# Kernel optimization log

Hardware: AMD Instinct MI355X
Metric: run time of the kernel (lower is better)

Reference implementation:

```python
import jax, jax.numpy as jnp
import numpy as np

N_NODES = 100000
N_EDGES = 3200000
HID = 32
N_LAYERS = 3
EDGE_DIM = 2
NODE_IN = 2          # [P, Q]
V_DIM = 2            # [V_mag, V_angle]
VH = V_DIM + HID     # 34, per-node feature fed to the GNN layer
MSG_IN = 2 * VH + EDGE_DIM   # 70
UPD_IN = VH + HID            # 66


def setup_inputs() -> dict:
    key = jax.random.key(0)
    ks = jax.random.split(key, 16)
    s = lambda *sh: 1.0 / np.sqrt(sh[-2]) if len(sh) >= 2 else 0.0
    inp = {
        "P_Q_inj": jax.random.normal(ks[0], (N_NODES, NODE_IN), dtype=jnp.float32),
        "senders": jax.random.randint(ks[1], (N_EDGES,), 0, N_NODES, dtype=jnp.int32),
        "receivers": jax.random.randint(ks[2], (N_EDGES,), 0, N_NODES, dtype=jnp.int32),
        "edge_features": jax.random.normal(ks[3], (N_EDGES, EDGE_DIM), dtype=jnp.float32),
        "edge_mask": jax.random.uniform(ks[4], (N_EDGES,), dtype=jnp.float32),
        # input embedding Dense(hidden_dim)
        "W_in": jax.random.normal(ks[5], (NODE_IN, HID), dtype=jnp.float32) * s(NODE_IN, HID),
        "b_in": jnp.zeros((HID,), dtype=jnp.float32),
        # per-layer params (flax compact loop -> distinct params per layer), stacked on axis 0
        "W_msg": jax.random.normal(ks[6], (N_LAYERS, MSG_IN, HID), dtype=jnp.float32) * s(MSG_IN, HID),
        "b_msg": jnp.zeros((N_LAYERS, HID), dtype=jnp.float32),
        "W_upd": jax.random.normal(ks[7], (N_LAYERS, UPD_IN, HID), dtype=jnp.float32) * s(UPD_IN, HID),
        "b_upd": jnp.zeros((N_LAYERS, HID), dtype=jnp.float32),
        "W_delta": jax.random.normal(ks[8], (N_LAYERS, HID, V_DIM), dtype=jnp.float32) * s(HID, V_DIM),
        "b_delta": jnp.zeros((N_LAYERS, V_DIM), dtype=jnp.float32),
    }
    return inp


def _layer(v, senders, receivers, edge_features, edge_mask, W_msg, b_msg, W_upd, b_upd):
    # v: [N, VH] node features. Gather sender/receiver feats, edge-wise MLP message,
    # soft mask, scatter-sum to receivers, then dense node update.
    msg_in = jnp.concatenate([v[senders], v[receivers], edge_features], axis=-1)  # [E, 70]
    m = jax.nn.relu(msg_in @ W_msg + b_msg)                                       # [E, H]
    m = m * edge_mask[:, None]
    agg = jax.ops.segment_sum(m, receivers, num_segments=v.shape[0])              # [N, H]
    v_out = jnp.concatenate([v, agg], axis=-1) @ W_upd + b_upd                    # [N, H]
    return v_out


def reference(P_Q_inj, senders, receivers, edge_features, edge_mask,
              W_in, b_in, W_msg, b_msg, W_upd, b_upd, W_delta, b_delta):
    V_pred = jnp.zeros_like(P_Q_inj).at[:, 0].set(1.0)   # [N, 2]
    h = P_Q_inj @ W_in + b_in                            # [N, H]
    for l in range(N_LAYERS):
        v_input = jnp.concatenate([V_pred, h], axis=-1)  # [N, 34]
        v_out = _layer(v_input, senders, receivers, edge_features, edge_mask,
                       W_msg[l], b_msg[l], W_upd[l], b_upd[l])
        h = jax.nn.relu(v_out)
        delta_V = h @ W_delta[l] + b_delta[l]
        V_pred = V_pred + delta_V
    return V_pred
```

## Files before the change

### kernel.cpp

```cpp
#include <hip/hip_runtime.h>
#include <hip/hip_fp16.h>

#define NN 100000
#define NE 3200000
#define NB 1563
#define NBLK ((NN + 255) / 256)
#define CHUNK 8192
#define NCH 391
#define CAP 4096

typedef float f32x4 __attribute__((ext_vector_type(4)));
typedef unsigned int u32x4 __attribute__((ext_vector_type(4)));

__device__ __forceinline__ float2 h2f2(unsigned int u) {
  __half2 h;
  *reinterpret_cast<unsigned int*>(&h) = u;
  return __half22float2(h);
}
__device__ __forceinline__ unsigned int f2h2(float x, float y) {
  __half2 h = __floats2half2_rn(x, y);
  return *reinterpret_cast<unsigned int*>(&h);
}


__global__ __launch_bounds__(1024) void k_hist(const int* __restrict__ recv, int* __restrict__ histmat) {
  __shared__ int h[NB];
  int t = threadIdx.x, c = blockIdx.x;
  for (int i = t; i < NB; i += 1024) h[i] = 0;
  __syncthreads();
  int start = c * CHUNK;
  int end = min(start + CHUNK, NE);
  for (int i = start + t; i < end; i += 1024)
    atomicAdd(&h[__builtin_nontemporal_load(recv + i) >> 6], 1);
  __syncthreads();
  for (int i = t; i < NB; i += 1024) histmat[c * NB + i] = h[i];
}


__global__ __launch_bounds__(256) void k_scanA(const int* __restrict__ histmat, int* __restrict__ total) {
  int b = blockIdx.x * 256 + threadIdx.x;
  if (b >= NB) return;
  int s = 0;
#pragma unroll 4
  for (int c = 0; c < NCH; c++) s += histmat[c * NB + b];
  total[b] = s;
}


__global__ __launch_bounds__(256) void k_scanB(const int* __restrict__ total, int* __restrict__ boff) {
  __shared__ int ps[256];
  int t = threadIdx.x;
  const int PER = (NB + 255) / 256;
  int v[PER];
  int s = 0;
#pragma unroll
  for (int k = 0; k < PER; k++) {
    int i = t * PER + k;
    v[k] = (i < NB) ? total[i] : 0;
    s += v[k];
  }
  ps[t] = s;
  __syncthreads();
  for (int o = 1; o < 256; o <<= 1) {
    int x = (t >= o) ? ps[t - o] : 0;
    __syncthreads();
    ps[t] += x;
    __syncthreads();
  }
  int run = (t > 0) ? ps[t - 1] : 0;
#pragma unroll
  for (int k = 0; k < PER; k++) {
    int i = t * PER + k;
    if (i < NB) {
      boff[i] = run;
      run += v[k];
    }
  }
  if (t == 255) boff[NB] = ps[255];
}


__global__ __launch_bounds__(256) void k_scanC(int* __restrict__ histmat, const int* __restrict__ boff) {
  int b = blockIdx.x * 256 + threadIdx.x;
  if (b >= NB) return;
  int run = boff[b];
#pragma unroll 4
  for (int c = 0; c < NCH; c++) {
    int v = histmat[c * NB + b];
    histmat[c * NB + b] = run;
    run += v;
  }
}


__global__ __launch_bounds__(1024) void k_scat(const int* __restrict__ send, const int* __restrict__ recv,
                                               const float2* __restrict__ ef, const float* __restrict__ mask,
                                               const int* __restrict__ boffc, float4* __restrict__ sorted) {
  __shared__ float4 stg[CHUNK];
  __shared__ unsigned short bkt[CHUNK];
  __shared__ int ofs[NB];
  __shared__ int cur[NB];
  __shared__ int wsum[16];
  int t = threadIdx.x, c = blockIdx.x;
  int start = c * CHUNK;
  int end = min(start + CHUNK, NE);
  int len = end - start;
  for (int i = t; i < NB; i += 1024) cur[i] = 0;
  __syncthreads();
  for (int i = start + t; i < end; i += 1024)
    atomicAdd(&cur[__builtin_nontemporal_load(recv + i) >> 6], 1);
  __syncthreads();
  int v0 = (2 * t < NB) ? cur[2 * t] : 0;
  int v1 = (2 * t + 1 < NB) ? cur[2 * t + 1] : 0;
  int s = v0 + v1;
  int lane = t & 63, wid = t >> 6;
  for (int o = 1; o < 64; o <<= 1) {
    int x = __shfl_up(s, o);
    if (lane >= o) s += x;
  }
  if (lane == 63) wsum[wid] = s;
  __syncthreads();
  if (wid == 0) {
    int ws = (lane < 16) ? wsum[lane] : 0;
    for (int o = 1; o < 16; o <<= 1) {
      int x = __shfl_up(ws, o);
      if (lane >= o) ws += x;
    }
    if (lane < 16) wsum[lane] = ws;
  }
  __syncthreads();
  int excl = s - v0 - v1 + ((wid > 0) ? wsum[wid - 1] : 0);
  __syncthreads();
  if (2 * t < NB) {
    cur[2 * t] = excl;
    ofs[2 * t] = boffc[c * NB + 2 * t] - excl;
  }
  if (2 * t + 1 < NB) {
    cur[2 * t + 1] = excl + v0;
    ofs[2 * t + 1] = boffc[c * NB + 2 * t + 1] - (excl + v0);
  }
  __syncthreads();
  for (int i = start + t; i < end; i += 1024) {
    int r = recv[i];
    int b = r >> 6;
    int p = atomicAdd(&cur[b], 1);
    float2 e2 = ef[i];
    float4 vv;
    vv.x = __int_as_float((send[i] << 6) | (r & 63));
    vv.y = e2.x;
    vv.z = e2.y;
    vv.w = mask[i];
    stg[p] = vv;
    bkt[p] = (unsigned short)b;
  }
  __syncthreads();
  for (int p = t; p < len; p += 1024) {
    int b = bkt[p];
    sorted[ofs[b] + p] = stg[p];
  }
}


__global__ __launch_bounds__(256) void k_bsort(const int* __restrict__ boff, float4* __restrict__ sorted,
                                               int* __restrict__ row_off) {
  __shared__ int cnt[4096];
  __shared__ int part[256];
  __shared__ float4 stg[CAP];
  int t = threadIdx.x, b = blockIdx.x;
  int base = boff[b], end = boff[b + 1];
  int Eb = end - base;
  int n0 = b * 64;
  for (int i = t; i < 4096; i += 256) cnt[i] = 0;
  __syncthreads();
  for (int e = base + t; e < end; e += 256) {
    int pk = __float_as_int(sorted[e].x);
    int key = ((pk & 63) << 6) | (pk >> 17);
    atomicAdd(&cnt[key], 1);
  }
  __syncthreads();
  int s = 0;
#pragma unroll
  for (int k = 0; k < 16; k++) s += cnt[t * 16 + k];
  part[t] = s;
  __syncthreads();
  for (int o = 1; o < 256; o <<= 1) {
    int x = (t >= o) ? part[t - o] : 0;
    __syncthreads();
    part[t] += x;
    __syncthreads();
  }
  int run = part[t] - s;
#pragma unroll
  for (int k = 0; k < 16; k++) {
    int c = cnt[t * 16 + k];
    cnt[t * 16 + k] = run;
    run += c;
  }
  __syncthreads();
  if (t < 64) {
    int n = n0 + t;
    if (n < NN) row_off[n] = base + cnt[t << 6];
  }
  if (b == NB - 1 && t == 0) row_off[NN] = end;
  __syncthreads();
  for (int e = base + t; e < end; e += 256) {
    float4 r = sorted[e];
    int pk = __float_as_int(r.x);
    int key = ((pk & 63) << 6) | (pk >> 17);
    int p = atomicAdd(&cnt[key], 1);
    stg[p] = r;
  }
  __syncthreads();
  for (int i = t; i < Eb; i += 256) sorted[base + i] = stg[i];
}


__global__ __launch_bounds__(256) void k_init(const float2* __restrict__ PQ,
                                              const float* __restrict__ Win, const float* __restrict__ bin,
                                              const float* __restrict__ Wm, const float* __restrict__ bm,
                                              float* __restrict__ h, __half* __restrict__ a,
                                              float* __restrict__ bp, float2* __restrict__ Vp) {
  int n = blockIdx.x * 256 + threadIdx.x;
  if (n >= NN) return;
  float2 pq = PQ[n];
  float hh[32];
#pragma unroll
  for (int j = 0; j < 32; j++) hh[j] = fmaf(pq.x, Win[j], fmaf(pq.y, Win[32 + j], bin[j]));
  float4* h4 = (float4*)(h + (size_t)n * 32);
#pragma unroll
  for (int j = 0; j < 8; j++) h4[j] = make_float4(hh[4*j], hh[4*j+1], hh[4*j+2], hh[4*j+3]);
  Vp[n] = make_float2(1.0f, 0.0f);
  float av[32], bv[32];
#pragma unroll
  for (int j = 0; j < 32; j++) { av[j] = Wm[j]; bv[j] = Wm[34 * 32 + j] + bm[j]; }
#pragma unroll 1
  for (int k = 0; k < 32; k++) {
    float hk = hh[k];
#pragma unroll
    for (int j = 0; j < 32; j++) {
      av[j] = fmaf(hk, Wm[(2 + k) * 32 + j], av[j]);
      bv[j] = fmaf(hk, Wm[(36 + k) * 32 + j], bv[j]);
    }
  }
  u32x4* dst = (u32x4*)(a + (size_t)n * 32);
#pragma unroll
  for (int g = 0; g < 4; g++) {
    u32x4 p;
    p.x = f2h2(av[g*8+0], av[g*8+1]);
    p.y = f2h2(av[g*8+2], av[g*8+3]);
    p.z = f2h2(av[g*8+4], av[g*8+5]);
    p.w = f2h2(av[g*8+6], av[g*8+7]);
    dst[g] = p;
  }
  float4* b4 = (float4*)(bp + (size_t)n * 32);
#pragma unroll
  for (int j = 0; j < 8; j++) b4[j] = make_float4(bv[4*j], bv[4*j+1], bv[4*j+2], bv[4*j+3]);
}


__global__ __launch_bounds__(256) void k_edge(const __half* __restrict__ a, const float* __restrict__ bp,
                                              const int* __restrict__ row_off, const f32x4* __restrict__ sorted,
                                              const float* __restrict__ Wm, float* __restrict__ agg) {
  int t = threadIdx.x;
  int n = blockIdx.x * 64 + (t >> 2);
  if (n >= NN) return;
  int ch = (t & 3) * 8;
  const float* wr = Wm + 68 * 32 + ch;
  float w0[8], w1[8];
#pragma unroll
  for (int j = 0; j < 8; j++) { w0[j] = wr[j]; w1[j] = wr[32 + j]; }
  const float4 bna = *(const float4*)(bp + (size_t)n * 32 + ch);
  const float4 bnb = *(const float4*)(bp + (size_t)n * 32 + ch + 4);
  float bn[8] = {bna.x, bna.y, bna.z, bna.w, bnb.x, bnb.y, bnb.z, bnb.w};
  float acc[8] = {0.f, 0.f, 0.f, 0.f, 0.f, 0.f, 0.f, 0.f};
  int e0 = row_off[n], e1 = row_off[n + 1];
  f32x4 rec = {0.f, 0.f, 0.f, 0.f};
  if (e0 < e1) rec = __builtin_nontemporal_load(sorted + e0);
#pragma unroll 2
  for (int e = e0; e < e1; ++e) {
    int pk = __float_as_int(rec.x);
    float c0 = rec.y, c1 = rec.z, mk = rec.w;
    const u32x4 pa = *(const u32x4*)(a + (size_t)(pk >> 6) * 32 + ch);
    if (e + 1 < e1) rec = __builtin_nontemporal_load(sorted + e + 1);
    float2 f0 = h2f2(pa.x), f1 = h2f2(pa.y), f2 = h2f2(pa.z), f3 = h2f2(pa.w);
    float av[8] = {f0.x, f0.y, f1.x, f1.y, f2.x, f2.y, f3.x, f3.y};
#pragma unroll
    for (int j = 0; j < 8; j++)
      acc[j] = fmaf(fmaxf(av[j] + fmaf(c0, w0[j], fmaf(c1, w1[j], bn[j])), 0.f), mk, acc[j]);
  }
  float* gp = agg + (size_t)n * 32 + ch;
  *(float4*)gp       = make_float4(acc[0], acc[1], acc[2], acc[3]);
  *(float4*)(gp + 4) = make_float4(acc[4], acc[5], acc[6], acc[7]);
}


__global__ __launch_bounds__(256) void k_node(const float* __restrict__ agg,
                                              const float* __restrict__ Wu, const float* __restrict__ bu,
                                              const float* __restrict__ Wd, const float* __restrict__ bd,
                                              const float* __restrict__ Wm, const float* __restrict__ bm,
                                              float* __restrict__ h, __half* __restrict__ a,
                                              float* __restrict__ bp, float2* __restrict__ Vp,
                                              float2* __restrict__ out, int last) {
  int n = blockIdx.x * 256 + threadIdx.x;
  if (n >= NN) return;
  float2 vp = Vp[n];
  float v0 = vp.x, v1 = vp.y;
  float hh[32], ag[32];
  const float4* h4 = (const float4*)(h + (size_t)n * 32);
  const float4* g4 = (const float4*)(agg + (size_t)n * 32);
#pragma unroll
  for (int jj = 0; jj < 8; jj++) {
    float4 x = h4[jj];
    hh[4*jj] = x.x; hh[4*jj+1] = x.y; hh[4*jj+2] = x.z; hh[4*jj+3] = x.w;
    float4 y = g4[jj];
    ag[4*jj] = y.x; ag[4*jj+1] = y.y; ag[4*jj+2] = y.z; ag[4*jj+3] = y.w;
  }
  float vo[32];
#pragma unroll
  for (int j = 0; j < 32; j++) vo[j] = fmaf(v0, Wu[j], fmaf(v1, Wu[32 + j], bu[j]));
#pragma unroll 1
  for (int k = 0; k < 32; k++) {
    float hk = hh[k], ak = ag[k];
#pragma unroll
    for (int j = 0; j < 32; j++) {
      vo[j] = fmaf(hk, Wu[(2 + k) * 32 + j], vo[j]);
      vo[j] = fmaf(ak, Wu[(34 + k) * 32 + j], vo[j]);
    }
  }
#pragma unroll
  for (int j = 0; j < 32; j++) hh[j] = fmaxf(vo[j], 0.0f);
  float d0 = bd[0], d1 = bd[1];
#pragma unroll 1
  for (int k = 0; k < 32; k++) {
    d0 = fmaf(hh[k], Wd[2 * k], d0);
    d1 = fmaf(hh[k], Wd[2 * k + 1], d1);
  }
  v0 += d0;
  v1 += d1;
  if (last) {
    out[n] = make_float2(v0, v1);
    return;
  }
  Vp[n] = make_float2(v0, v1);
  float4* hw4 = (float4*)(h + (size_t)n * 32);
#pragma unroll
  for (int jj = 0; jj < 8; jj++) hw4[jj] = make_float4(hh[4*jj], hh[4*jj+1], hh[4*jj+2], hh[4*jj+3]);
  float av[32], bv[32];
#pragma unroll
  for (int j = 0; j < 32; j++) {
    av[j] = fmaf(v0, Wm[j], v1 * Wm[32 + j]);
    bv[j] = fmaf(v0, Wm[34 * 32 + j], fmaf(v1, Wm[35 * 32 + j], bm[j]));
  }
#pragma unroll 1
  for (int k = 0; k < 32; k++) {
    float hk = hh[k];
#pragma unroll
    for (int j = 0; j < 32; j++) {
      av[j] = fmaf(hk, Wm[(2 + k) * 32 + j], av[j]);
      bv[j] = fmaf(hk, Wm[(36 + k) * 32 + j], bv[j]);
    }
  }
  u32x4* dst = (u32x4*)(a + (size_t)n * 32);
#pragma unroll
  for (int g = 0; g < 4; g++) {
    u32x4 p;
    p.x = f2h2(av[g*8+0], av[g*8+1]);
    p.y = f2h2(av[g*8+2], av[g*8+3]);
    p.z = f2h2(av[g*8+4], av[g*8+5]);
    p.w = f2h2(av[g*8+6], av[g*8+7]);
    dst[g] = p;
  }
  float4* b4 = (float4*)(bp + (size_t)n * 32);
#pragma unroll
  for (int jj = 0; jj < 8; jj++) b4[jj] = make_float4(bv[4*jj], bv[4*jj+1], bv[4*jj+2], bv[4*jj+3]);
}


extern "C" void kernel_launch(void* const* d_in, const int* in_sizes, int n_in,
                              void* d_out, int out_size, void* d_ws, size_t ws_size,
                              hipStream_t stream) {
  const float* PQ   = (const float*)d_in[0];
  const int*   send = (const int*)d_in[1];
  const int*   recv = (const int*)d_in[2];
  const float* ef   = (const float*)d_in[3];
  const float* mask = (const float*)d_in[4];
  const float* Win  = (const float*)d_in[5];
  const float* bin  = (const float*)d_in[6];
  const float* Wmsg = (const float*)d_in[7];
  const float* bmsg = (const float*)d_in[8];
  const float* Wupd = (const float*)d_in[9];
  const float* bupd = (const float*)d_in[10];
  const float* Wdel = (const float*)d_in[11];
  const float* bdel = (const float*)d_in[12];
  float2* out = (float2*)d_out;

  char* w = (char*)d_ws;
  auto alloc = [&](size_t bytes) {
    char* p = w;
    w += (bytes + 255) & ~(size_t)255;
    return p;
  };
  float4* sorted = (float4*)alloc((size_t)NE * 16);
  int* histmat = (int*)alloc((size_t)NCH * NB * 4);
  int* total   = (int*)alloc((size_t)NB * 4);
  int* boff    = (int*)alloc(((size_t)NB + 1) * 4);
  int* row_off = (int*)alloc(((size_t)NN + 1) * 4);
  float* h    = (float*)alloc((size_t)NN * 32 * 4);
  __half* a   = (__half*)alloc((size_t)NN * 32 * 2);
  float* bp   = (float*)alloc((size_t)NN * 32 * 4);
  float* agg  = (float*)alloc((size_t)NN * 32 * 4);
  float2* Vp  = (float2*)alloc((size_t)NN * 8);

  k_hist<<<NCH, 1024, 0, stream>>>(recv, histmat);
  k_scanA<<<(NB + 255) / 256, 256, 0, stream>>>(histmat, total);
  k_scanB<<<1, 256, 0, stream>>>(total, boff);
  k_scanC<<<(NB + 255) / 256, 256, 0, stream>>>(histmat, boff);
  k_scat<<<NCH, 1024, 0, stream>>>(send, recv, (const float2*)ef, mask, histmat, sorted);
  k_bsort<<<NB, 256, 0, stream>>>(boff, sorted, row_off);

  k_init<<<NBLK, 256, 0, stream>>>((const float2*)PQ, Win, bin, Wmsg, bmsg, h, a, bp, Vp);

  for (int l = 0; l < 3; l++) {
    int last = (l == 2) ? 1 : 0;
    int lnext = (l + 1) % 3;
    k_edge<<<NB, 256, 0, stream>>>(a, bp, row_off, (const f32x4*)sorted, Wmsg + l * 70 * 32, agg);
    k_node<<<NBLK, 256, 0, stream>>>(agg, Wupd + l * 66 * 32, bupd + l * 32,
                                     Wdel + l * 64, bdel + l * 2,
                                     Wmsg + lnext * 70 * 32, bmsg + lnext * 32,
                                     h, a, bp, Vp, out, last);
  }
}
```

Measured before the change: 577.6 us.

## Halve threads per node in edge kernel and software-pipeline gathers two edges ahead

The edge-aggregation kernel now assigns two threads per receiver node (16 channels each) instead of four (8 channels each), so each sorted edge record is loaded by half as many threads. The loop also prefetches edge records three ahead and the gathered fp16 sender features two edges ahead, which aims to hide gather latency. Launch bounds now request 4 blocks per CU and the grid shrinks accordingly. The costs are higher register pressure from 16-wide accumulators and weights plus the prefetch buffers, and fewer total threads available to hide latency.

```diff
diff --git a/kernel.cpp b/kernel.cpp
--- a/kernel.cpp
+++ b/kernel.cpp
@@ -8,6 +8,7 @@
 #define CHUNK 8192
 #define NCH 391
 #define CAP 4096
+#define EBK ((NN + 127) / 128)
 
 typedef float f32x4 __attribute__((ext_vector_type(4)));
 typedef unsigned int u32x4 __attribute__((ext_vector_type(4)));
@@ -258,39 +259,69 @@
 }
 
 
-__global__ __launch_bounds__(256) void k_edge(const __half* __restrict__ a, const float* __restrict__ bp,
-                                              const int* __restrict__ row_off, const f32x4* __restrict__ sorted,
-                                              const float* __restrict__ Wm, float* __restrict__ agg) {
+__global__ __launch_bounds__(256, 4) void k_edge(const __half* __restrict__ a, const float* __restrict__ bp,
+                                                 const int* __restrict__ row_off, const f32x4* __restrict__ sorted,
+                                                 const float* __restrict__ Wm, float* __restrict__ agg) {
   int t = threadIdx.x;
-  int n = blockIdx.x * 64 + (t >> 2);
+  int n = blockIdx.x * 128 + (t >> 1);
   if (n >= NN) return;
-  int ch = (t & 3) * 8;
+  int ch = (t & 1) * 16;
   const float* wr = Wm + 68 * 32 + ch;
-  float w0[8], w1[8];
-#pragma unroll
-  for (int j = 0; j < 8; j++) { w0[j] = wr[j]; w1[j] = wr[32 + j]; }
-  const float4 bna = *(const float4*)(bp + (size_t)n * 32 + ch);
-  const float4 bnb = *(const float4*)(bp + (size_t)n * 32 + ch + 4);
-  float bn[8] = {bna.x, bna.y, bna.z, bna.w, bnb.x, bnb.y, bnb.z, bnb.w};
-  float acc[8] = {0.f, 0.f, 0.f, 0.f, 0.f, 0.f, 0.f, 0.f};
+  float w0[16], w1[16];
+#pragma unroll
+  for (int j = 0; j < 16; j++) { w0[j] = wr[j]; w1[j] = wr[32 + j]; }
+  float bn[16];
+  const float4* bq = (const float4*)(bp + (size_t)n * 32 + ch);
+#pragma unroll
+  for (int q = 0; q < 4; q++) {
+    float4 bv = bq[q];
+    bn[4*q] = bv.x; bn[4*q+1] = bv.y; bn[4*q+2] = bv.z; bn[4*q+3] = bv.w;
+  }
+  float acc[16];
+#pragma unroll
+  for (int j = 0; j < 16; j++) acc[j] = 0.f;
+  const __half* abase = a + ch;
   int e0 = row_off[n], e1 = row_off[n + 1];
-  f32x4 rec = {0.f, 0.f, 0.f, 0.f};
-  if (e0 < e1) rec = __builtin_nontemporal_load(sorted + e0);
-#pragma unroll 2
+  f32x4 r0 = {0,0,0,0}, r1 = {0,0,0,0}, r2 = {0,0,0,0};
+  u32x4 gA0 = {0,0,0,0}, gA1 = {0,0,0,0}, gB0 = {0,0,0,0}, gB1 = {0,0,0,0};
+  if (e0 < e1)     r0 = __builtin_nontemporal_load(sorted + e0);
+  if (e0 + 1 < e1) r1 = __builtin_nontemporal_load(sorted + e0 + 1);
+  if (e0 + 2 < e1) r2 = __builtin_nontemporal_load(sorted + e0 + 2);
+  if (e0 < e1) {
+    const __half* ap = abase + (size_t)(__float_as_int(r0.x) >> 6) * 32;
+    gA0 = *(const u32x4*)ap;
+    gA1 = *(const u32x4*)(ap + 8);
+  }
+  if (e0 + 1 < e1) {
+    const __half* ap = abase + (size_t)(__float_as_int(r1.x) >> 6) * 32;
+    gB0 = *(const u32x4*)ap;
+    gB1 = *(const u32x4*)(ap + 8);
+  }
   for (int e = e0; e < e1; ++e) {
-    int pk = __float_as_int(rec.x);
-    float c0 = rec.y, c1 = rec.z, mk = rec.w;
-    const u32x4 pa = *(const u32x4*)(a + (size_t)(pk >> 6) * 32 + ch);
-    if (e + 1 < e1) rec = __builtin_nontemporal_load(sorted + e + 1);
-    float2 f0 = h2f2(pa.x), f1 = h2f2(pa.y), f2 = h2f2(pa.z), f3 = h2f2(pa.w);
-    float av[8] = {f0.x, f0.y, f1.x, f1.y, f2.x, f2.y, f3.x, f3.y};
-#pragma unroll
-    for (int j = 0; j < 8; j++)
+    f32x4 rc = r0;
+    u32x4 q0 = gA0, q1 = gA1;
+    r0 = r1; r1 = r2;
+    gA0 = gB0; gA1 = gB1;
+    if (e + 3 < e1) r2 = __builtin_nontemporal_load(sorted + e + 3);
+    if (e + 2 < e1) {
+      const __half* ap = abase + (size_t)(__float_as_int(r1.x) >> 6) * 32;
+      gB0 = *(const u32x4*)ap;
+      gB1 = *(const u32x4*)(ap + 8);
+    }
+    float c0 = rc.y, c1 = rc.z, mk = rc.w;
+    float2 f0 = h2f2(q0.x), f1 = h2f2(q0.y), f2 = h2f2(q0.z), f3 = h2f2(q0.w);
+    float2 f4 = h2f2(q1.x), f5 = h2f2(q1.y), f6 = h2f2(q1.z), f7 = h2f2(q1.w);
+    float av[16] = {f0.x, f0.y, f1.x, f1.y, f2.x, f2.y, f3.x, f3.y,
+                    f4.x, f4.y, f5.x, f5.y, f6.x, f6.y, f7.x, f7.y};
+#pragma unroll
+    for (int j = 0; j < 16; j++)
       acc[j] = fmaf(fmaxf(av[j] + fmaf(c0, w0[j], fmaf(c1, w1[j], bn[j])), 0.f), mk, acc[j]);
   }
   float* gp = agg + (size_t)n * 32 + ch;
-  *(float4*)gp       = make_float4(acc[0], acc[1], acc[2], acc[3]);
-  *(float4*)(gp + 4) = make_float4(acc[4], acc[5], acc[6], acc[7]);
+  *(float4*)gp        = make_float4(acc[0],  acc[1],  acc[2],  acc[3]);
+  *(float4*)(gp + 4)  = make_float4(acc[4],  acc[5],  acc[6],  acc[7]);
+  *(float4*)(gp + 8)  = make_float4(acc[8],  acc[9],  acc[10], acc[11]);
+  *(float4*)(gp + 12) = make_float4(acc[12], acc[13], acc[14], acc[15]);
 }
 
 
@@ -423,7 +454,7 @@
   for (int l = 0; l < 3; l++) {
     int last = (l == 2) ? 1 : 0;
     int lnext = (l + 1) % 3;
-    k_edge<<<NB, 256, 0, stream>>>(a, bp, row_off, (const f32x4*)sorted, Wmsg + l * 70 * 32, agg);
+    k_edge<<<EBK, 256, 0, stream>>>(a, bp, row_off, (const f32x4*)sorted, Wmsg + l * 70 * 32, agg);
     k_node<<<NBLK, 256, 0, stream>>>(agg, Wupd + l * 66 * 32, bupd + l * 32,
                                      Wdel + l * 64, bdel + l * 2,
                                      Wmsg + lnext * 70 * 32, bmsg + lnext * 32,
```

Measured after the change: 596.1 us. +3.2%, slower.
